# Kernel optimization log

Hardware: AMD Instinct MI355X
Metric: run time of the kernel (lower is better)

Reference implementation:

```python
import jax, jax.numpy as jnp
import numpy as np

N_EMBED = 1024
HEAD_SIZE = 128
B, T = 8, 2048


def setup_inputs() -> dict:
    key = jax.random.key(0)
    kx, kk, kq, kv = jax.random.split(key, 4)
    x = jax.random.normal(kx, (B, T, N_EMBED), dtype=jnp.float32)
    Wk = jax.random.normal(kk, (N_EMBED, HEAD_SIZE), dtype=jnp.float32) * (N_EMBED ** -0.5)
    Wq = jax.random.normal(kq, (N_EMBED, HEAD_SIZE), dtype=jnp.float32) * (N_EMBED ** -0.5)
    Wv = jax.random.normal(kv, (N_EMBED, HEAD_SIZE), dtype=jnp.float32) * (N_EMBED ** -0.5)
    return {"x": x, "Wk": Wk, "Wq": Wq, "Wv": Wv}


def reference(x, Wk, Wq, Wv):
    # x: [B, T, C]; single-head causal attention, dropout rate 0 (identity)
    t = x.shape[1]
    k = jnp.einsum("btc,ch->bth", x, Wk)  # keys
    q = jnp.einsum("btc,ch->bth", x, Wq)  # queries
    v = jnp.einsum("btc,ch->bth", x, Wv)  # values
    scale = k.shape[-1] ** -0.5
    scores = jnp.einsum("bqh,bkh->bqk", q, k) * scale  # [B, T, T]
    causal = jnp.tril(jnp.ones((t, t), dtype=bool))
    scores = jnp.where(causal, scores, -jnp.inf)
    attn = jax.nn.softmax(scores, axis=-1)
    return jnp.einsum("bqk,bkh->bqh", attn, v)
```

## Files before the change

### kernel.cpp

```cpp
#include <hip/hip_runtime.h>
#include <hip/hip_bf16.h>
#include <math.h>

#define B_ 8
#define T_ 2048
#define C_ 1024
#define D_ 128
#define M_ (B_*T_)

typedef __attribute__((ext_vector_type(8))) short short8;
typedef __attribute__((ext_vector_type(4))) float floatx4;
typedef __hip_bfloat16 bf16;

#define QSCALE 0.12751744416218247f

__global__ __launch_bounds__(256) void cvt_w3_kernel(const float* __restrict__ Wq,
                                                     const float* __restrict__ Wk,
                                                     const float* __restrict__ Wv,
                                                     bf16* __restrict__ Wt2) {
    __shared__ bf16 tl[64][136];
    const int t = threadIdx.x;
    const int kc = blockIdx.x, g = blockIdx.y;
    const int k0 = kc * 64;
    const float* W = (g == 0) ? Wq : (g == 1) ? Wk : Wv;
    {
        int k = t >> 2, n0 = (t & 3) * 32;
        const float* src = W + (size_t)(k0 + k) * 128 + n0;
#pragma unroll
        for (int j = 0; j < 4; ++j) {
            float4 v0 = *(const float4*)(src + j * 8);
            float4 v1 = *(const float4*)(src + j * 8 + 4);
            union { short8 s; __hip_bfloat162 h[4]; } u;
            __hip_bfloat162 h;
            h.x = __float2bfloat16(v0.x); h.y = __float2bfloat16(v0.y); u.h[0] = h;
            h.x = __float2bfloat16(v0.z); h.y = __float2bfloat16(v0.w); u.h[1] = h;
            h.x = __float2bfloat16(v1.x); h.y = __float2bfloat16(v1.y); u.h[2] = h;
            h.x = __float2bfloat16(v1.z); h.y = __float2bfloat16(v1.w); u.h[3] = h;
            *(short8*)&tl[k][n0 + j * 8] = u.s;
        }
    }
    __syncthreads();
    {
#pragma unroll
        for (int j = 0; j < 4; ++j) {
            int cid = t + j * 256;
            int lane = cid & 63, dk = (cid >> 6) & 1, cb = cid >> 7;
            int krow = dk * 32 + (lane >> 4) * 8;
            int ncol = cb * 16 + (lane & 15);
            union { short8 s; bf16 e[8]; } u;
#pragma unroll
            for (int e = 0; e < 8; ++e) u.e[e] = tl[krow + e][ncol];
            bf16* dst = Wt2 + ((((size_t)(g * 8 + cb) * 16 + kc) * 2 + dk) * 64 + lane) * 8;
            *(short8*)dst = u.s;
        }
    }
}

__global__ __launch_bounds__(512, 2) void proj10_kernel(const float* __restrict__ x,
                                                        const bf16* __restrict__ Wt2,
                                                        bf16* __restrict__ Qb,
                                                        bf16* __restrict__ Kb,
                                                        bf16* __restrict__ Vt) {
    __shared__ bf16 smem[2 * 64 * 72];
    const int t = threadIdx.x;
    const int wave = t >> 6, lane = t & 63;
    const int quad = lane >> 4, l15 = lane & 15;
    const int row0 = blockIdx.x * 64;
    const int xrow = t >> 3, xc8 = (t & 7) * 8;
    const float* xbase = x + (size_t)(row0 + xrow) * 1024 + xc8;
    const bf16* wbase = Wt2 + (size_t)lane * 8;

    floatx4 acc[4][3];
#pragma unroll
    for (int m = 0; m < 4; ++m)
#pragma unroll
        for (int n = 0; n < 3; ++n) acc[m][n] = (floatx4)0.0f;

    float4 xr0, xr1;
    short8 br[6];

    xr0 = *(const float4*)xbase;
    xr1 = *(const float4*)(xbase + 4);
    {
        union { short8 s; __hip_bfloat162 h[4]; } u;
        __hip_bfloat162 h;
        h.x = __float2bfloat16(xr0.x); h.y = __float2bfloat16(xr0.y); u.h[0] = h;
        h.x = __float2bfloat16(xr0.z); h.y = __float2bfloat16(xr0.w); u.h[1] = h;
        h.x = __float2bfloat16(xr1.x); h.y = __float2bfloat16(xr1.y); u.h[2] = h;
        h.x = __float2bfloat16(xr1.z); h.y = __float2bfloat16(xr1.w); u.h[3] = h;
        *(short8*)&smem[xrow * 72 + xc8] = u.s;
    }
    xr0 = *(const float4*)(xbase + 64);
    xr1 = *(const float4*)(xbase + 68);
#pragma unroll
    for (int n = 0; n < 3; ++n)
#pragma unroll
        for (int dk = 0; dk < 2; ++dk)
            br[dk * 3 + n] = *(const short8*)(wbase + ((size_t)((wave * 3 + n) * 16 + 0) * 1024 + dk * 512));

    for (int kc = 0; kc < 16; ++kc) {
        __syncthreads();
        short8 brn[6];
        if (kc < 15) {
#pragma unroll
            for (int n = 0; n < 3; ++n)
#pragma unroll
                for (int dk = 0; dk < 2; ++dk)
                    brn[dk * 3 + n] = *(const short8*)(wbase + ((size_t)((wave * 3 + n) * 16 + kc + 1) * 1024 + dk * 512));
            union { short8 s; __hip_bfloat162 h[4]; } u;
            __hip_bfloat162 h;
            h.x = __float2bfloat16(xr0.x); h.y = __float2bfloat16(xr0.y); u.h[0] = h;
            h.x = __float2bfloat16(xr0.z); h.y = __float2bfloat16(xr0.w); u.h[1] = h;
            h.x = __float2bfloat16(xr1.x); h.y = __float2bfloat16(xr1.y); u.h[2] = h;
            h.x = __float2bfloat16(xr1.z); h.y = __float2bfloat16(xr1.w); u.h[3] = h;
            *(short8*)&smem[((kc + 1) & 1) * 4608 + xrow * 72 + xc8] = u.s;
        }
        if (kc < 14) {
            const float* s = xbase + (kc + 2) * 64;
            xr0 = *(const float4*)s;
            xr1 = *(const float4*)(s + 4);
        }
        const bf16* lc = smem + (kc & 1) * 4608;
#pragma unroll
        for (int dk = 0; dk < 2; ++dk) {
            short8 af[4];
#pragma unroll
            for (int m = 0; m < 4; ++m)
                af[m] = *(const short8*)&lc[(m * 16 + l15) * 72 + dk * 32 + quad * 8];
#pragma unroll
            for (int m = 0; m < 4; ++m)
#pragma unroll
                for (int n = 0; n < 3; ++n)
                    acc[m][n] = __builtin_amdgcn_mfma_f32_16x16x32_bf16(af[m], br[dk * 3 + n], acc[m][n], 0, 0, 0);
        }
        if (kc < 15) {
#pragma unroll
            for (int i = 0; i < 6; ++i) br[i] = brn[i];
        }
    }

    __syncthreads();
    bf16* vtl = smem;
#pragma unroll
    for (int m = 0; m < 4; ++m)
#pragma unroll
        for (int r = 0; r < 4; ++r) {
            const int tt = m * 16 + quad * 4 + r;
            const int row = row0 + tt;
#pragma unroll
            for (int n = 0; n < 3; ++n) {
                const int colb = wave * 48 + n * 16;
                const int g = colb >> 7;
                const int lc_ = (colb & 127) + l15;
                const float v = acc[m][n][r];
                if (g == 0)      Qb[(size_t)row * 128 + lc_] = __float2bfloat16(v * QSCALE);
                else if (g == 1) Kb[(size_t)row * 128 + lc_] = __float2bfloat16(v);
                else             vtl[tt * 137 + lc_] = __float2bfloat16(v);
            }
        }
    __syncthreads();
    {
        int d = t >> 2, toff = (t & 3) * 16;
        union { short8 s[2]; bf16 e[16]; } u;
#pragma unroll
        for (int i = 0; i < 16; ++i) u.e[i] = vtl[(toff + i) * 137 + d];
        int bb = row0 >> 11, t0 = row0 & 2047;
        bf16* dst = Vt + (size_t)(bb * D_ + d) * T_ + t0 + toff;
        *(short8*)dst       = u.s[0];
        *(short8*)(dst + 8) = u.s[1];
    }
}

__global__ __launch_bounds__(512, 4) void flash_fm4_kernel(const bf16* __restrict__ Qb,
                                                           const bf16* __restrict__ Kb,
                                                           const bf16* __restrict__ Vt,
                                                           float* __restrict__ out,
                                                           bf16* __restrict__ Opart,
                                                           float* __restrict__ Lpart) {
    const int tile = blockIdx.x, seg = blockIdx.y, b = blockIdx.z;
    const int keys_total = (tile + 1) * 128;
    const int nseg = (keys_total + 511) >> 9;
    if (seg >= nseg) return;

    __shared__ bf16 lds_k[64][136];
    __shared__ bf16 lds_v[128][72];
    __shared__ bf16 lds_p[8][16][72];
    const int t = threadIdx.x;
    const int wave = t >> 6, lane = t & 63;
    const int quad = lane >> 4, l15 = lane & 15;
    const int q0 = tile * 128;
    const int k_start = seg << 9;
    const int k_end = min(k_start + 512, keys_total);
    const int nch = (k_end - k_start) >> 6;

    short8 qf[4];
    {
        int qm = q0 + wave * 16 + l15;
#pragma unroll
        for (int dk = 0; dk < 4; ++dk)
            qf[dk] = *(const short8*)(Qb + (size_t)(b * T_ + qm) * 128 + dk * 32 + quad * 8);
    }

    short8 kreg[2], vreg[2];
    {
        const int k0 = k_start;
#pragma unroll
        for (int j = 0; j < 2; ++j) {
            int c = t + j * 512;
            { int r = c >> 4, co = (c & 15) * 8;
              kreg[j] = *(const short8*)(Kb + (size_t)(b * T_ + k0 + r) * 128 + co); }
            { int d = c >> 3, co = (c & 7) * 8;
              vreg[j] = *(const short8*)(Vt + (size_t)b * (D_ * T_) + d * T_ + k0 + co); }
        }
    }

    floatx4 o_acc[8];
#pragma unroll
    for (int i = 0; i < 8; ++i) o_acc[i] = (floatx4)0.0f;
    float lp[4] = {0.f, 0.f, 0.f, 0.f};
    const int qrow = q0 + wave * 16 + quad * 4;

    for (int ch = 0; ch < nch; ++ch) {
        const int k0 = k_start + (ch << 6);
        __syncthreads();
#pragma unroll
        for (int j = 0; j < 2; ++j) {
            int c = t + j * 512;
            { int r = c >> 4, co = (c & 15) * 8; *(short8*)&lds_k[r][co] = kreg[j]; }
            { int d = c >> 3, co = (c & 7) * 8;  *(short8*)&lds_v[d][co] = vreg[j]; }
        }
        if (ch + 1 < nch) {
            const int kn = k0 + 64;
#pragma unroll
            for (int j = 0; j < 2; ++j) {
                int c = t + j * 512;
                { int r = c >> 4, co = (c & 15) * 8;
                  kreg[j] = *(const short8*)(Kb + (size_t)(b * T_ + kn + r) * 128 + co); }
                { int d = c >> 3, co = (c & 7) * 8;
                  vreg[j] = *(const short8*)(Vt + (size_t)b * (D_ * T_) + d * T_ + kn + co); }
            }
        }
        __syncthreads();

        floatx4 s[4];
#pragma unroll
        for (int nt = 0; nt < 4; ++nt) s[nt] = (floatx4)0.0f;
#pragma unroll
        for (int dk = 0; dk < 4; ++dk)
#pragma unroll
            for (int nt = 0; nt < 4; ++nt) {
                short8 kb = *(const short8*)&lds_k[nt * 16 + l15][dk * 32 + quad * 8];
                s[nt] = __builtin_amdgcn_mfma_f32_16x16x32_bf16(qf[dk], kb, s[nt], 0, 0, 0);
            }

        float sv[4][4];
#pragma unroll
        for (int nt = 0; nt < 4; ++nt)
#pragma unroll
            for (int r = 0; r < 4; ++r) sv[nt][r] = s[nt][r];

        if (k0 + 63 > qrow) {
#pragma unroll
            for (int nt = 0; nt < 4; ++nt) {
                int key = k0 + nt * 16 + l15;
#pragma unroll
                for (int r = 0; r < 4; ++r)
                    if (key > qrow + r) sv[nt][r] = -1e30f;
            }
        }

#pragma unroll
        for (int nt = 0; nt < 4; ++nt)
#pragma unroll
            for (int r = 0; r < 4; ++r) sv[nt][r] = exp2f(sv[nt][r]);
#pragma unroll
        for (int r = 0; r < 4; ++r)
            lp[r] += (sv[0][r] + sv[1][r]) + (sv[2][r] + sv[3][r]);

#pragma unroll
        for (int nt = 0; nt < 4; ++nt)
#pragma unroll
            for (int r = 0; r < 4; ++r)
                lds_p[wave][quad * 4 + r][nt * 16 + l15] = __float2bfloat16(sv[nt][r]);
        short8 pa0 = *(const short8*)&lds_p[wave][l15][quad * 8];
        short8 pa1 = *(const short8*)&lds_p[wave][l15][32 + quad * 8];

#pragma unroll
        for (int nt = 0; nt < 8; ++nt) {
            short8 vb0 = *(const short8*)&lds_v[nt * 16 + l15][quad * 8];
            short8 vb1 = *(const short8*)&lds_v[nt * 16 + l15][32 + quad * 8];
            o_acc[nt] = __builtin_amdgcn_mfma_f32_16x16x32_bf16(pa0, vb0, o_acc[nt], 0, 0, 0);
            o_acc[nt] = __builtin_amdgcn_mfma_f32_16x16x32_bf16(pa1, vb1, o_acc[nt], 0, 0, 0);
        }
    }

    float l_i[4];
#pragma unroll
    for (int r = 0; r < 4; ++r) {
        float v = lp[r];
        v += __shfl_xor(v, 1);
        v += __shfl_xor(v, 2);
        v += __shfl_xor(v, 4);
        v += __shfl_xor(v, 8);
        l_i[r] = v;
    }

    const int lrow = wave * 16 + quad * 4;
    if (nseg == 1) {
        float inv_l[4];
#pragma unroll
        for (int r = 0; r < 4; ++r) inv_l[r] = 1.0f / l_i[r];
#pragma unroll
        for (int f = 0; f < 8; ++f)
#pragma unroll
            for (int r = 0; r < 4; ++r)
                out[(size_t)(b * T_ + qrow + r) * 128 + f * 16 + l15] = o_acc[f][r] * inv_l[r];
    } else {
        int pre = 0;
        for (int u = 4; u < tile; ++u) pre += (u + 4) >> 2;
        const size_t slot = (size_t)b * 36 + pre + seg;
        bf16* ob = Opart + slot * (128 * 128);
#pragma unroll
        for (int f = 0; f < 8; ++f)
#pragma unroll
            for (int r = 0; r < 4; ++r)
                ob[(size_t)(lrow + r) * 128 + f * 16 + l15] = __float2bfloat16(o_acc[f][r]);
        if (l15 == 0) {
#pragma unroll
            for (int r = 0; r < 4; ++r)
                Lpart[slot * 128 + lrow + r] = l_i[r];
        }
    }
}

__global__ __launch_bounds__(256) void combine6_kernel(const bf16* __restrict__ Opart,
                                                       const float* __restrict__ Lpart,
                                                       float* __restrict__ out) {
    const int tile = blockIdx.x + 4, b = blockIdx.y;
    const int nseg = (tile + 4) >> 2;
    int pre = 0;
    for (int u = 4; u < tile; ++u) pre += (u + 4) >> 2;
    const size_t slot0 = (size_t)b * 36 + pre;
    const int t = threadIdx.x;
    const int row = t >> 1, c0 = (t & 1) * 64;

    float lsum = 0.f;
    for (int j = 0; j < nseg; ++j) lsum += Lpart[(slot0 + j) * 128 + row];

    float acc[64];
#pragma unroll
    for (int i = 0; i < 64; ++i) acc[i] = 0.f;
    for (int j = 0; j < nseg; ++j) {
        const bf16* src = Opart + (slot0 + j) * (128 * 128) + (size_t)row * 128 + c0;
#pragma unroll
        for (int u = 0; u < 8; ++u) {
            short8 v8 = *(const short8*)(src + u * 8);
#pragma unroll
            for (int e = 0; e < 8; ++e) {
                union { unsigned int u32; float f; } cv;
                cv.u32 = ((unsigned int)(unsigned short)v8[e]) << 16;
                acc[u * 8 + e] += cv.f;
            }
        }
    }
    float inv = 1.0f / lsum;
    float* dst = out + (size_t)(b * T_ + tile * 128 + row) * 128 + c0;
#pragma unroll
    for (int i = 0; i < 64; ++i) dst[i] = acc[i] * inv;
}

extern "C" void kernel_launch(void* const* d_in, const int* in_sizes, int n_in,
                              void* d_out, int out_size, void* d_ws, size_t ws_size,
                              hipStream_t stream) {
    const float* x  = (const float*)d_in[0];
    const float* Wk = (const float*)d_in[1];
    const float* Wq = (const float*)d_in[2];
    const float* Wv = (const float*)d_in[3];
    float* out = (float*)d_out;

    char* ws = (char*)d_ws;
    bf16*  Wt2   = (bf16*)ws;
    bf16*  Qb    = (bf16*)(ws + 786432);
    bf16*  Kb    = (bf16*)(ws + 4980736);
    bf16*  Vt    = (bf16*)(ws + 9175040);
    bf16*  Opart = (bf16*)(ws + 13369344);
    float* Lpart = (float*)(ws + 31719424);

    cvt_w3_kernel<<<dim3(16, 3), 256, 0, stream>>>(Wq, Wk, Wv, Wt2);
    proj10_kernel<<<256, 512, 0, stream>>>(x, Wt2, Qb, Kb, Vt);
    flash_fm4_kernel<<<dim3(16, 4, B_), 512, 0, stream>>>(Qb, Kb, Vt, out, Opart, Lpart);
    combine6_kernel<<<dim3(12, B_), 256, 0, stream>>>(Opart, Lpart, out);
}
```

Measured before the change: 76.39 us.

## Rewrite QKV projection with direct global-to-LDS loads and triple-buffered pipeline

The projection kernel now uses global_load_lds to stream both fp32 x tiles and bf16 weight tiles straight into LDS through a three-stage buffer ring with explicit vmcnt waits. The bf16 conversion of x moves to the point where fragments are read from LDS, and the LDS layout uses an XOR swizzle. The grid doubles to 512 blocks by splitting the 384 output columns into two groups, with a remapped block index. The goal is to overlap loads with MFMA work and to remove register staging. In exchange, each x tile is loaded twice (once per column group), LDS use grows to 60KB, and the hand-counted vmcnt waits are fragile.

```diff
diff --git a/kernel.cpp b/kernel.cpp
--- a/kernel.cpp
+++ b/kernel.cpp
@@ -13,6 +13,10 @@
 typedef __hip_bfloat16 bf16;
 
 #define QSCALE 0.12751744416218247f
+
+#define GLDS16(gsrc, ldst) \
+    __builtin_amdgcn_global_load_lds((const __attribute__((address_space(1))) unsigned int*)(gsrc), \
+                                     (__attribute__((address_space(3))) unsigned int*)(ldst), 16, 0, 0)
 
 __global__ __launch_bounds__(256) void cvt_w3_kernel(const float* __restrict__ Wq,
                                                      const float* __restrict__ Wk,
@@ -56,110 +60,130 @@
     }
 }
 
-__global__ __launch_bounds__(512, 2) void proj10_kernel(const float* __restrict__ x,
+__global__ __launch_bounds__(512, 2) void proj21_kernel(const float* __restrict__ x,
                                                         const bf16* __restrict__ Wt2,
                                                         bf16* __restrict__ Qb,
                                                         bf16* __restrict__ Kb,
                                                         bf16* __restrict__ Vt) {
-    __shared__ bf16 smem[2 * 64 * 72];
+    __shared__ __attribute__((aligned(16))) char smem[61440];
     const int t = threadIdx.x;
     const int wave = t >> 6, lane = t & 63;
     const int quad = lane >> 4, l15 = lane & 15;
-    const int row0 = blockIdx.x * 64;
-    const int xrow = t >> 3, xc8 = (t & 7) * 8;
-    const float* xbase = x + (size_t)(row0 + xrow) * 1024 + xc8;
-    const bf16* wbase = Wt2 + (size_t)lane * 8;
-
-    floatx4 acc[4][3];
-#pragma unroll
-    for (int m = 0; m < 4; ++m)
+    const int wr = wave >> 2, wc = wave & 3;
+    const int phys = blockIdx.x;
+    const int lb = (phys & 7) * 64 + (phys >> 3);
+    const int rt = lb >> 1, cg = lb & 1;
+    const int row0 = rt * 64;
+
+    const bf16* wsrc0;
+    const bf16* wsrc1;
+    int wc0lds, wc1lds;
+    if (wave < 4) {
+        const int c0 = wave * 2, c1 = wave * 2 + 1;
+        wsrc0 = Wt2 + (size_t)(cg * 12 + c0) * 16384 + lane * 8;
+        wsrc1 = Wt2 + (size_t)(cg * 12 + c1) * 16384 + lane * 8;
+        wc0lds = c0 * 1024; wc1lds = c1 * 1024;
+    } else {
+        const int c0 = wave + 4;
+        wsrc0 = Wt2 + (size_t)(cg * 12 + c0) * 16384 + lane * 8;
+        wsrc1 = wsrc0; wc0lds = c0 * 1024; wc1lds = -1;
+    }
+    const float* xsrc = x + (size_t)(row0 + wave * 8 + (lane >> 3)) * 1024
+                          + ((lane & 7) ^ (lane >> 3)) * 4;
+
+    floatx4 acc[2][3];
+#pragma unroll
+    for (int m = 0; m < 2; ++m)
 #pragma unroll
         for (int n = 0; n < 3; ++n) acc[m][n] = (floatx4)0.0f;
 
-    float4 xr0, xr1;
-    short8 br[6];
-
-    xr0 = *(const float4*)xbase;
-    xr1 = *(const float4*)(xbase + 4);
-    {
-        union { short8 s; __hip_bfloat162 h[4]; } u;
-        __hip_bfloat162 h;
-        h.x = __float2bfloat16(xr0.x); h.y = __float2bfloat16(xr0.y); u.h[0] = h;
-        h.x = __float2bfloat16(xr0.z); h.y = __float2bfloat16(xr0.w); u.h[1] = h;
-        h.x = __float2bfloat16(xr1.x); h.y = __float2bfloat16(xr1.y); u.h[2] = h;
-        h.x = __float2bfloat16(xr1.z); h.y = __float2bfloat16(xr1.w); u.h[3] = h;
-        *(short8*)&smem[xrow * 72 + xc8] = u.s;
-    }
-    xr0 = *(const float4*)(xbase + 64);
-    xr1 = *(const float4*)(xbase + 68);
-#pragma unroll
-    for (int n = 0; n < 3; ++n)
-#pragma unroll
-        for (int dk = 0; dk < 2; ++dk)
-            br[dk * 3 + n] = *(const short8*)(wbase + ((size_t)((wave * 3 + n) * 16 + 0) * 1024 + dk * 512));
-
-    for (int kc = 0; kc < 16; ++kc) {
+#define ISSUE(S_, BUF_)                                                           \
+    {                                                                             \
+        char* wd = smem + (BUF_) * 12288;                                         \
+        char* xd = smem + 36864 + (BUF_) * 8192;                                  \
+        GLDS16(wsrc0 + (size_t)(S_) * 512, wd + wc0lds);                          \
+        if (wave < 4) GLDS16(wsrc1 + (size_t)(S_) * 512, wd + wc1lds);            \
+        GLDS16(xsrc + (size_t)(S_) * 32, xd + wave * 1024);                       \
+    }
+
+#define COMPUTE(S_, BUF_)                                                         \
+    {                                                                             \
+        const char* wb = smem + (BUF_) * 12288;                                   \
+        const char* xb = smem + 36864 + (BUF_) * 8192;                            \
+        short8 af[2], bff[3];                                                     \
+        _Pragma("unroll")                                                         \
+        for (int m = 0; m < 2; ++m) {                                             \
+            const int r = wr * 32 + m * 16 + l15;                                 \
+            const int r7 = r & 7;                                                 \
+            float4 a0 = *(const float4*)(xb + r * 128 + (((2 * quad) ^ r7) * 16));\
+            float4 a1 = *(const float4*)(xb + r * 128 + (((2 * quad + 1) ^ r7) * 16));\
+            union { short8 s8; __hip_bfloat162 h[4]; } u;                         \
+            __hip_bfloat162 hh;                                                   \
+            hh.x = __float2bfloat16(a0.x); hh.y = __float2bfloat16(a0.y); u.h[0] = hh;\
+            hh.x = __float2bfloat16(a0.z); hh.y = __float2bfloat16(a0.w); u.h[1] = hh;\
+            hh.x = __float2bfloat16(a1.x); hh.y = __float2bfloat16(a1.y); u.h[2] = hh;\
+            hh.x = __float2bfloat16(a1.z); hh.y = __float2bfloat16(a1.w); u.h[3] = hh;\
+            af[m] = u.s8;                                                         \
+        }                                                                         \
+        _Pragma("unroll")                                                         \
+        for (int n = 0; n < 3; ++n)                                               \
+            bff[n] = *(const short8*)(wb + (wc * 3 + n) * 1024 + lane * 16);      \
+        __builtin_amdgcn_s_setprio(1);                                            \
+        _Pragma("unroll")                                                         \
+        for (int m = 0; m < 2; ++m)                                               \
+            _Pragma("unroll")                                                     \
+            for (int n = 0; n < 3; ++n)                                           \
+                acc[m][n] = __builtin_amdgcn_mfma_f32_16x16x32_bf16(af[m], bff[n],\
+                                                              acc[m][n], 0, 0, 0);\
+        __builtin_amdgcn_s_setprio(0);                                            \
+    }
+
+    ISSUE(0, 0)
+    ISSUE(1, 1)
+    if (wave < 4) asm volatile("s_waitcnt vmcnt(3)" ::: "memory");
+    else          asm volatile("s_waitcnt vmcnt(2)" ::: "memory");
+    __builtin_amdgcn_s_barrier();
+
+    int bcur = 0;
+    for (int s = 0; s < 32; ++s) {
+        const int bnext2 = (bcur + 2 >= 3) ? bcur - 1 : bcur + 2;
+        if (s < 30) ISSUE(s + 2, bnext2)
+        COMPUTE(s, bcur)
+        if (s < 31) {
+            if (s < 30) {
+                if (wave < 4) asm volatile("s_waitcnt vmcnt(3)" ::: "memory");
+                else          asm volatile("s_waitcnt vmcnt(2)" ::: "memory");
+            } else {
+                asm volatile("s_waitcnt vmcnt(0)" ::: "memory");
+            }
+            __builtin_amdgcn_s_barrier();
+        }
+        bcur = (bcur + 1 == 3) ? 0 : bcur + 1;
+    }
+#undef ISSUE
+#undef COMPUTE
+
+    __syncthreads();
+    bf16* vtl = (bf16*)smem;
+#pragma unroll
+    for (int m = 0; m < 2; ++m)
+#pragma unroll
+        for (int r = 0; r < 4; ++r) {
+            const int tt = wr * 32 + m * 16 + quad * 4 + r;
+            const int row = row0 + tt;
+#pragma unroll
+            for (int n = 0; n < 3; ++n) {
+                const int colb = cg * 192 + wc * 48 + n * 16;
+                const int g = colb >> 7;
+                const int lc = (colb & 127) + l15;
+                const float v = acc[m][n][r];
+                if (g == 0)      Qb[(size_t)row * 128 + lc] = __float2bfloat16(v * QSCALE);
+                else if (g == 1) Kb[(size_t)row * 128 + lc] = __float2bfloat16(v);
+                else             vtl[tt * 137 + lc] = __float2bfloat16(v);
+            }
+        }
+    if (cg == 1) {
         __syncthreads();
-        short8 brn[6];
-        if (kc < 15) {
-#pragma unroll
-            for (int n = 0; n < 3; ++n)
-#pragma unroll
-                for (int dk = 0; dk < 2; ++dk)
-                    brn[dk * 3 + n] = *(const short8*)(wbase + ((size_t)((wave * 3 + n) * 16 + kc + 1) * 1024 + dk * 512));
-            union { short8 s; __hip_bfloat162 h[4]; } u;
-            __hip_bfloat162 h;
-            h.x = __float2bfloat16(xr0.x); h.y = __float2bfloat16(xr0.y); u.h[0] = h;
-            h.x = __float2bfloat16(xr0.z); h.y = __float2bfloat16(xr0.w); u.h[1] = h;
-            h.x = __float2bfloat16(xr1.x); h.y = __float2bfloat16(xr1.y); u.h[2] = h;
-            h.x = __float2bfloat16(xr1.z); h.y = __float2bfloat16(xr1.w); u.h[3] = h;
-            *(short8*)&smem[((kc + 1) & 1) * 4608 + xrow * 72 + xc8] = u.s;
-        }
-        if (kc < 14) {
-            const float* s = xbase + (kc + 2) * 64;
-            xr0 = *(const float4*)s;
-            xr1 = *(const float4*)(s + 4);
-        }
-        const bf16* lc = smem + (kc & 1) * 4608;
-#pragma unroll
-        for (int dk = 0; dk < 2; ++dk) {
-            short8 af[4];
-#pragma unroll
-            for (int m = 0; m < 4; ++m)
-                af[m] = *(const short8*)&lc[(m * 16 + l15) * 72 + dk * 32 + quad * 8];
-#pragma unroll
-            for (int m = 0; m < 4; ++m)
-#pragma unroll
-                for (int n = 0; n < 3; ++n)
-                    acc[m][n] = __builtin_amdgcn_mfma_f32_16x16x32_bf16(af[m], br[dk * 3 + n], acc[m][n], 0, 0, 0);
-        }
-        if (kc < 15) {
-#pragma unroll
-            for (int i = 0; i < 6; ++i) br[i] = brn[i];
-        }
-    }
-
-    __syncthreads();
-    bf16* vtl = smem;
-#pragma unroll
-    for (int m = 0; m < 4; ++m)
-#pragma unroll
-        for (int r = 0; r < 4; ++r) {
-            const int tt = m * 16 + quad * 4 + r;
-            const int row = row0 + tt;
-#pragma unroll
-            for (int n = 0; n < 3; ++n) {
-                const int colb = wave * 48 + n * 16;
-                const int g = colb >> 7;
-                const int lc_ = (colb & 127) + l15;
-                const float v = acc[m][n][r];
-                if (g == 0)      Qb[(size_t)row * 128 + lc_] = __float2bfloat16(v * QSCALE);
-                else if (g == 1) Kb[(size_t)row * 128 + lc_] = __float2bfloat16(v);
-                else             vtl[tt * 137 + lc_] = __float2bfloat16(v);
-            }
-        }
-    __syncthreads();
-    {
         int d = t >> 2, toff = (t & 3) * 16;
         union { short8 s[2]; bf16 e[16]; } u;
 #pragma unroll
@@ -387,7 +411,7 @@
     float* Lpart = (float*)(ws + 31719424);
 
     cvt_w3_kernel<<<dim3(16, 3), 256, 0, stream>>>(Wq, Wk, Wv, Wt2);
-    proj10_kernel<<<256, 512, 0, stream>>>(x, Wt2, Qb, Kb, Vt);
+    proj21_kernel<<<512, 512, 0, stream>>>(x, Wt2, Qb, Kb, Vt);
     flash_fm4_kernel<<<dim3(16, 4, B_), 512, 0, stream>>>(Qb, Kb, Vt, out, Opart, Lpart);
     combine6_kernel<<<dim3(12, B_), 256, 0, stream>>>(Opart, Lpart, out);
 }
```

After: 77.56 us. About the same (+1.5%).
